# Performance work log

Measured on AMD Instinct MI355X. Metric: run time of the kernel, lower is better.

## Reference

```python
import jax, jax.numpy as jnp
import numpy as np

B, T, E, K, NNEG = 128, 512, 128, 4, 64


def setup_inputs() -> dict:
    key = jax.random.key(0)
    k1, k2, k3, k4 = jax.random.split(key, 4)
    base_payload = jax.random.normal(k1, (B, T, E), dtype=jnp.float32)
    mapped_ctx_payload = jax.random.normal(k2, (B, T, E, K), dtype=jnp.float32)
    seq_lens = jax.random.randint(k3, (B,), 1, T + 1, dtype=jnp.int32)
    # valid positions mask over the flattened (B*T) pool of possible negatives
    valid = (jnp.arange(T)[None, :] < seq_lens[:, None]).reshape(-1)  # [B*T]
    logits = jnp.where(valid, 0.0, -1e30)[None, :]                    # [1, B*T]
    logits = jnp.broadcast_to(logits, (B, B * T))
    # mirrors torch.multinomial(mask, n_negatives): one draw set per batch row
    sample_ids = jax.random.categorical(k4, logits, shape=(NNEG, B)).T.astype(jnp.int32)
    return {
        "base_payload": base_payload,
        "mapped_ctx_payload": mapped_ctx_payload,
        "seq_lens": seq_lens,
        "sample_ids": sample_ids,
    }


def reference(base_payload, mapped_ctx_payload, seq_lens, sample_ids):
    b, t, e = base_payload.shape
    n_steps = mapped_ctx_payload.shape[-1]
    # length mask [b, t]
    len_mask = (jnp.arange(t)[None, :] < seq_lens[:, None]).astype(base_payload.dtype)
    # zero context embeddings past each sequence's length
    trimmed_mce = mapped_ctx_payload * len_mask[:, :, None, None]  # [b, t, e, n_steps]
    # gather sampled negatives from the flattened base embedding pool
    neg_samples = base_payload.reshape(b * t, e)[sample_ids]  # [b, n_neg, e]

    step_losses = []
    for i in range(1, n_steps + 1):
        ce_i = trimmed_mce[:, : t - i, :, i - 1]   # [b, t-i, e]
        be_i = base_payload[:, i:]                  # [b, t-i, e]
        positive_pred = jnp.sum(ce_i * be_i, axis=-1)             # [b, t-i]
        neg_pred = jnp.einsum('bse,bne->bsn', ce_i, neg_samples)  # [b, t-i, n_neg]
        logits = jnp.concatenate([positive_pred[..., None], neg_pred], axis=-1)
        step_losses.append(-jax.nn.log_softmax(logits, axis=-1)[:, :, 0].mean())
    return jnp.stack(step_losses).mean()
```

## Files before the change

### kernel.cpp

```cpp
#include <hip/hip_runtime.h>
#include <math.h>

#define NB 128
#define NT 512
#define NEDIM 128
#define NNEG 64
#define SCHUNK 32
#define NBLK (NB * (NT / SCHUNK))

typedef __bf16 bf16x8 __attribute__((ext_vector_type(8)));
typedef float  f32x4  __attribute__((ext_vector_type(4)));

__launch_bounds__(256, 3)
__global__ void cpc_mfma_kernel(const float* __restrict__ base,
                                const float* __restrict__ mce,
                                const int*  __restrict__ seq_lens,
                                const int*  __restrict__ sample_ids,
                                float* __restrict__ ws)
{
    const int b    = blockIdx.y;
    const int s0   = blockIdx.x * SCHUNK;
    const int slot = b * (NT / SCHUNK) + blockIdx.x;
    const int L    = seq_lens[b];
    const float LOG65 = 4.1743873f;
    const float wgt[4] = {1.f/261632.f, 1.f/261120.f, 1.f/260608.f, 1.f/260096.f};

    if (s0 >= L) {
        if (threadIdx.x == 0) {
            float c = 0.f;
            #pragma unroll
            for (int i = 1; i <= 4; ++i) {
                int hi = min(SCHUNK, (NT - i) - s0);
                if (hi > 0) c += (float)hi * LOG65 * wgt[i - 1];
            }
            ws[slot] = c;
        }
        return;
    }

    __shared__ __bf16 Afrag[2048 * 8];
    __shared__ __bf16 Bfrag[1024 * 8];
    __shared__ float  pos_lds[128];
    __shared__ float  wsum[4];

    const int tid  = threadIdx.x;
    const int lane = tid & 63;
    const int w    = tid >> 6;
    const int q    = lane >> 4;
    const int fl   = lane & 15;

    const float4* mce4 = (const float4*)mce;

    #pragma unroll
    for (int it = 0; it < 2; ++it) {
        int g  = tid + 256 * it;
        int s  = g & 31;
        int eb = g >> 5;
        const float4* src = mce4 + (size_t)(b * NT + s0 + s) * NEDIM + eb * 8;
        float4 v[8];
        #pragma unroll
        for (int u = 0; u < 8; ++u) v[u] = src[u];
        const float* vf = (const float*)v;
        int Cs = (eb >> 2) * 8 + (s >> 2);
        int base_chunk = Cs * 64 + (eb & 3) * 16 + (s & 3) * 4;
        int x = Cs & 7;
        #pragma unroll
        for (int k = 0; k < 4; ++k) {
            int phys = (base_chunk + k) ^ x;
            bf16x8 o;
            #pragma unroll
            for (int u = 0; u < 8; ++u) o[u] = (__bf16)vf[4 * u + k];
            *(bf16x8*)(&Afrag[phys * 8]) = o;
        }
    }

    {
        int n = tid & 63;
        int r = sample_ids[b * NNEG + n];
        const float4* srcb = (const float4*)(base + (size_t)r * NEDIM);
        int eb0 = (tid >> 6) * 4;
        #pragma unroll
        for (int it = 0; it < 4; ++it) {
            int eb = eb0 + it;
            float4 v0 = srcb[eb * 2], v1 = srcb[eb * 2 + 1];
            const float* f0 = (const float*)&v0;
            const float* f1 = (const float*)&v1;
            bf16x8 o;
            #pragma unroll
            for (int u = 0; u < 4; ++u) { o[u] = (__bf16)f0[u]; o[4 + u] = (__bf16)f1[u]; }
            *(bf16x8*)(&Bfrag[(eb * 64 + n) * 8]) = o;
        }
    }
    __syncthreads();

    f32x4 acc[2][4];
    #pragma unroll
    for (int mtl = 0; mtl < 2; ++mtl)
        #pragma unroll
        for (int nt = 0; nt < 4; ++nt) acc[mtl][nt] = (f32x4){0.f, 0.f, 0.f, 0.f};

    #pragma unroll
    for (int kstep = 0; kstep < 4; ++kstep) {
        bf16x8 af[2];
        #pragma unroll
        for (int mtl = 0; mtl < 2; ++mtl) {
            int Cs = kstep * 8 + (2 * w + mtl);
            int phys = (Cs * 64 + lane) ^ (Cs & 7);
            af[mtl] = *(const bf16x8*)(&Afrag[phys * 8]);
        }
        bf16x8 bv[4];
        #pragma unroll
        for (int nt = 0; nt < 4; ++nt) {
            int cB = (kstep * 4 + q) * 64 + nt * 16 + fl;
            bv[nt] = *(const bf16x8*)(&Bfrag[cB * 8]);
        }
        #pragma unroll
        for (int mtl = 0; mtl < 2; ++mtl)
            #pragma unroll
            for (int nt = 0; nt < 4; ++nt)
                acc[mtl][nt] = __builtin_amdgcn_mfma_f32_16x16x32_bf16(
                    af[mtl], bv[nt], acc[mtl][nt], 0, 0, 0);
    }

    {
        int m    = tid >> 1;
        int eh   = tid & 1;
        int sloc = m >> 2, ip = (m & 3) + 1;
        int srow = s0 + sloc + ip; if (srow > NT - 1) srow = NT - 1;
        const float4* brow4 = (const float4*)(base + (size_t)(b * NT + srow) * NEDIM + eh * 64);
        int mt = m >> 4, flm = m & 15;
        float psum = 0.f;
        #pragma unroll
        for (int el = 0; el < 8; ++el) {
            int eb = eh * 8 + el;
            int Cs = (eb >> 2) * 8 + mt;
            int phys = (Cs * 64 + (eb & 3) * 16 + flm) ^ (Cs & 7);
            bf16x8 av = *(const bf16x8*)(&Afrag[phys * 8]);
            float4 b0 = brow4[el * 2], b1 = brow4[el * 2 + 1];
            const float* f0 = (const float*)&b0;
            const float* f1 = (const float*)&b1;
            #pragma unroll
            for (int u = 0; u < 4; ++u) {
                psum = fmaf((float)av[u],     f0[u], psum);
                psum = fmaf((float)av[4 + u], f1[u], psum);
            }
        }
        psum += __shfl_xor(psum, 1);
        if (eh == 0) pos_lds[m] = psum;
    }
    __syncthreads();

    float lossacc = 0.f;
    #pragma unroll
    for (int mtl = 0; mtl < 2; ++mtl) {
        #pragma unroll
        for (int r = 0; r < 4; ++r) {
            int m  = w * 32 + mtl * 16 + q * 4 + r;
            int sg = s0 + (m >> 2);
            int ip = (m & 3) + 1;
            float z0 = acc[mtl][0][r], z1 = acc[mtl][1][r];
            float z2 = acc[mtl][2][r], z3 = acc[mtl][3][r];
            float p  = pos_lds[m];
            float mx = fmaxf(fmaxf(z0, z1), fmaxf(z2, z3));
            mx = fmaxf(mx, __shfl_xor(mx, 1));
            mx = fmaxf(mx, __shfl_xor(mx, 2));
            mx = fmaxf(mx, __shfl_xor(mx, 4));
            mx = fmaxf(mx, __shfl_xor(mx, 8));
            mx = fmaxf(mx, p);
            float es = __expf(z0 - mx) + __expf(z1 - mx)
                     + __expf(z2 - mx) + __expf(z3 - mx);
            es += __shfl_xor(es, 1);
            es += __shfl_xor(es, 2);
            es += __shfl_xor(es, 4);
            es += __shfl_xor(es, 8);
            es += __expf(p - mx);
            float loss = __logf(es) + (mx - p);
            loss = (sg < L) ? loss : LOG65;
            bool take = (sg < NT - ip) && (fl == 0);
            lossacc += take ? wgt[ip - 1] * loss : 0.f;
        }
    }
    lossacc += __shfl_xor(lossacc, 16);
    lossacc += __shfl_xor(lossacc, 32);
    if (lane == 0) wsum[w] = lossacc;
    __syncthreads();
    if (tid == 0) ws[slot] = wsum[0] + wsum[1] + wsum[2] + wsum[3];
}

__global__ void reduce_k(const float* __restrict__ ws, float* __restrict__ out) {
    const int tid = threadIdx.x;
    float s = 0.f;
    #pragma unroll
    for (int i = 0; i < NBLK / 256; ++i) s += ws[tid + 256 * i];
    s += __shfl_xor(s, 1);
    s += __shfl_xor(s, 2);
    s += __shfl_xor(s, 4);
    s += __shfl_xor(s, 8);
    s += __shfl_xor(s, 16);
    s += __shfl_xor(s, 32);
    __shared__ float wsum[4];
    if ((tid & 63) == 0) wsum[tid >> 6] = s;
    __syncthreads();
    if (tid == 0) out[0] = wsum[0] + wsum[1] + wsum[2] + wsum[3];
}

extern "C" void kernel_launch(void* const* d_in, const int* in_sizes, int n_in,
                              void* d_out, int out_size, void* d_ws, size_t ws_size,
                              hipStream_t stream) {
    (void)in_sizes; (void)n_in; (void)out_size; (void)ws_size;
    const float* base       = (const float*)d_in[0];
    const float* mce        = (const float*)d_in[1];
    const int*   seq_lens   = (const int*)d_in[2];
    const int*   sample_ids = (const int*)d_in[3];
    float* out = (float*)d_out;
    float* ws  = (float*)d_ws;

    dim3 grid(NT / SCHUNK, NB);
    cpc_mfma_kernel<<<grid, 256, 0, stream>>>(base, mce, seq_lens, sample_ids, ws);
    reduce_k<<<1, 256, 0, stream>>>(ws, out);
}
```

Measured before the change: 222.8 us.

## Fold positive dot products into MFMA via extra shifted-row B columns

Measured after the change: 211.9 us. 4.9% less time.

```diff
diff --git a/kernel.cpp b/kernel.cpp
--- a/kernel.cpp
+++ b/kernel.cpp
@@ -5,13 +5,15 @@
 #define NT 512
 #define NEDIM 128
 #define NNEG 64
-#define SCHUNK 32
-#define NBLK (NB * (NT / SCHUNK))
+#define SCHUNK 16
+#define NCHUNK (NT / SCHUNK)
+#define NBLK (NB * NCHUNK)
+#define WSN (NBLK * 4)
 
 typedef __bf16 bf16x8 __attribute__((ext_vector_type(8)));
 typedef float  f32x4  __attribute__((ext_vector_type(4)));
 
-__launch_bounds__(256, 3)
+__launch_bounds__(256, 4)
 __global__ void cpc_mfma_kernel(const float* __restrict__ base,
                                 const float* __restrict__ mce,
                                 const int*  __restrict__ seq_lens,
@@ -20,28 +22,26 @@
 {
     const int b    = blockIdx.y;
     const int s0   = blockIdx.x * SCHUNK;
-    const int slot = b * (NT / SCHUNK) + blockIdx.x;
+    const int slot = (b * NCHUNK + blockIdx.x) * 4;
     const int L    = seq_lens[b];
     const float LOG65 = 4.1743873f;
     const float wgt[4] = {1.f/261632.f, 1.f/261120.f, 1.f/260608.f, 1.f/260096.f};
 
     if (s0 >= L) {
-        if (threadIdx.x == 0) {
+        if (threadIdx.x < 4) {
             float c = 0.f;
             #pragma unroll
             for (int i = 1; i <= 4; ++i) {
                 int hi = min(SCHUNK, (NT - i) - s0);
                 if (hi > 0) c += (float)hi * LOG65 * wgt[i - 1];
             }
-            ws[slot] = c;
+            ws[slot + threadIdx.x] = (threadIdx.x == 0) ? c : 0.f;
         }
         return;
     }
 
-    __shared__ __bf16 Afrag[2048 * 8];
-    __shared__ __bf16 Bfrag[1024 * 8];
-    __shared__ float  pos_lds[128];
-    __shared__ float  wsum[4];
+    __shared__ __bf16 Afrag[1024 * 8];
+    __shared__ __bf16 Bfrag[1536 * 8];
 
     const int tid  = threadIdx.x;
     const int lane = tid & 63;
@@ -51,17 +51,15 @@
 
     const float4* mce4 = (const float4*)mce;
 
-    #pragma unroll
-    for (int it = 0; it < 2; ++it) {
-        int g  = tid + 256 * it;
-        int s  = g & 31;
-        int eb = g >> 5;
+    {
+        int s  = tid & 15;
+        int eb = tid >> 4;
         const float4* src = mce4 + (size_t)(b * NT + s0 + s) * NEDIM + eb * 8;
         float4 v[8];
         #pragma unroll
         for (int u = 0; u < 8; ++u) v[u] = src[u];
         const float* vf = (const float*)v;
-        int Cs = (eb >> 2) * 8 + (s >> 2);
+        int Cs = (eb >> 2) * 4 + (s >> 2);
         int base_chunk = Cs * 64 + (eb & 3) * 16 + (s & 3) * 4;
         int x = Cs & 7;
         #pragma unroll
@@ -74,124 +72,103 @@
         }
     }
 
-    {
-        int n = tid & 63;
-        int r = sample_ids[b * NNEG + n];
+    #pragma unroll
+    for (int it = 0; it < 4; ++it) {
+        int h  = tid + 256 * it;
+        int n  = h >> 4;
+        int eb = h & 15;
+        int r  = sample_ids[b * NNEG + n];
         const float4* srcb = (const float4*)(base + (size_t)r * NEDIM);
-        int eb0 = (tid >> 6) * 4;
+        float4 v0 = srcb[eb * 2], v1 = srcb[eb * 2 + 1];
+        const float* f0 = (const float*)&v0;
+        const float* f1 = (const float*)&v1;
+        bf16x8 o;
         #pragma unroll
-        for (int it = 0; it < 4; ++it) {
-            int eb = eb0 + it;
-            float4 v0 = srcb[eb * 2], v1 = srcb[eb * 2 + 1];
+        for (int u = 0; u < 4; ++u) { o[u] = (__bf16)f0[u]; o[4 + u] = (__bf16)f1[u]; }
+        int phys = (eb * 96 + n) ^ (eb & 7);
+        *(bf16x8*)(&Bfrag[phys * 8]) = o;
+    }
+
+    #pragma unroll
+    for (int it = 0; it < 2; ++it) {
+        int h  = tid + 256 * it;
+        int j  = h >> 4;
+        int eb = h & 15;
+        bf16x8 o;
+        #pragma unroll
+        for (int u = 0; u < 8; ++u) o[u] = (__bf16)0.f;
+        if (j < SCHUNK + 3) {
+            int srow = s0 + 1 + j; if (srow > NT - 1) srow = NT - 1;
+            const float4* srcp = (const float4*)(base + (size_t)(b * NT + srow) * NEDIM);
+            float4 v0 = srcp[eb * 2], v1 = srcp[eb * 2 + 1];
             const float* f0 = (const float*)&v0;
             const float* f1 = (const float*)&v1;
-            bf16x8 o;
             #pragma unroll
             for (int u = 0; u < 4; ++u) { o[u] = (__bf16)f0[u]; o[4 + u] = (__bf16)f1[u]; }
-            *(bf16x8*)(&Bfrag[(eb * 64 + n) * 8]) = o;
         }
+        int phys = (eb * 96 + 64 + j) ^ (eb & 7);
+        *(bf16x8*)(&Bfrag[phys * 8]) = o;
     }
     __syncthreads();
 
-    f32x4 acc[2][4];
+    f32x4 acc[6];
     #pragma unroll
-    for (int mtl = 0; mtl < 2; ++mtl)
-        #pragma unroll
-        for (int nt = 0; nt < 4; ++nt) acc[mtl][nt] = (f32x4){0.f, 0.f, 0.f, 0.f};
+    for (int nt = 0; nt < 6; ++nt) acc[nt] = (f32x4){0.f, 0.f, 0.f, 0.f};
 
     #pragma unroll
     for (int kstep = 0; kstep < 4; ++kstep) {
-        bf16x8 af[2];
+        int CsA = kstep * 4 + w;
+        bf16x8 af = *(const bf16x8*)(&Afrag[((CsA * 64 + lane) ^ (CsA & 7)) * 8]);
+        int ebB = kstep * 4 + q;
+        int xb  = ebB & 7;
+        bf16x8 bv[6];
         #pragma unroll
-        for (int mtl = 0; mtl < 2; ++mtl) {
-            int Cs = kstep * 8 + (2 * w + mtl);
-            int phys = (Cs * 64 + lane) ^ (Cs & 7);
-            af[mtl] = *(const bf16x8*)(&Afrag[phys * 8]);
-        }
-        bf16x8 bv[4];
+        for (int nt = 0; nt < 6; ++nt)
+            bv[nt] = *(const bf16x8*)(&Bfrag[((ebB * 96 + nt * 16 + fl) ^ xb) * 8]);
         #pragma unroll
-        for (int nt = 0; nt < 4; ++nt) {
-            int cB = (kstep * 4 + q) * 64 + nt * 16 + fl;
-            bv[nt] = *(const bf16x8*)(&Bfrag[cB * 8]);
-        }
-        #pragma unroll
-        for (int mtl = 0; mtl < 2; ++mtl)
-            #pragma unroll
-            for (int nt = 0; nt < 4; ++nt)
-                acc[mtl][nt] = __builtin_amdgcn_mfma_f32_16x16x32_bf16(
-                    af[mtl], bv[nt], acc[mtl][nt], 0, 0, 0);
+        for (int nt = 0; nt < 6; ++nt)
+            acc[nt] = __builtin_amdgcn_mfma_f32_16x16x32_bf16(af, bv[nt], acc[nt], 0, 0, 0);
     }
 
-    {
-        int m    = tid >> 1;
-        int eh   = tid & 1;
-        int sloc = m >> 2, ip = (m & 3) + 1;
-        int srow = s0 + sloc + ip; if (srow > NT - 1) srow = NT - 1;
-        const float4* brow4 = (const float4*)(base + (size_t)(b * NT + srow) * NEDIM + eh * 64);
-        int mt = m >> 4, flm = m & 15;
-        float psum = 0.f;
-        #pragma unroll
-        for (int el = 0; el < 8; ++el) {
-            int eb = eh * 8 + el;
-            int Cs = (eb >> 2) * 8 + mt;
-            int phys = (Cs * 64 + (eb & 3) * 16 + flm) ^ (Cs & 7);
-            bf16x8 av = *(const bf16x8*)(&Afrag[phys * 8]);
-            float4 b0 = brow4[el * 2], b1 = brow4[el * 2 + 1];
-            const float* f0 = (const float*)&b0;
-            const float* f1 = (const float*)&b1;
-            #pragma unroll
-            for (int u = 0; u < 4; ++u) {
-                psum = fmaf((float)av[u],     f0[u], psum);
-                psum = fmaf((float)av[4 + u], f1[u], psum);
-            }
-        }
-        psum += __shfl_xor(psum, 1);
-        if (eh == 0) pos_lds[m] = psum;
-    }
-    __syncthreads();
-
+    const int sloc = w * 4 + q;
+    const int sg   = s0 + sloc;
     float lossacc = 0.f;
     #pragma unroll
-    for (int mtl = 0; mtl < 2; ++mtl) {
-        #pragma unroll
-        for (int r = 0; r < 4; ++r) {
-            int m  = w * 32 + mtl * 16 + q * 4 + r;
-            int sg = s0 + (m >> 2);
-            int ip = (m & 3) + 1;
-            float z0 = acc[mtl][0][r], z1 = acc[mtl][1][r];
-            float z2 = acc[mtl][2][r], z3 = acc[mtl][3][r];
-            float p  = pos_lds[m];
-            float mx = fmaxf(fmaxf(z0, z1), fmaxf(z2, z3));
-            mx = fmaxf(mx, __shfl_xor(mx, 1));
-            mx = fmaxf(mx, __shfl_xor(mx, 2));
-            mx = fmaxf(mx, __shfl_xor(mx, 4));
-            mx = fmaxf(mx, __shfl_xor(mx, 8));
-            mx = fmaxf(mx, p);
-            float es = __expf(z0 - mx) + __expf(z1 - mx)
-                     + __expf(z2 - mx) + __expf(z3 - mx);
-            es += __shfl_xor(es, 1);
-            es += __shfl_xor(es, 2);
-            es += __shfl_xor(es, 4);
-            es += __shfl_xor(es, 8);
-            es += __expf(p - mx);
-            float loss = __logf(es) + (mx - p);
-            loss = (sg < L) ? loss : LOG65;
-            bool take = (sg < NT - ip) && (fl == 0);
-            lossacc += take ? wgt[ip - 1] * loss : 0.f;
-        }
+    for (int r = 0; r < 4; ++r) {
+        int ip   = r + 1;
+        int pcol = sloc + r;
+        float z0 = acc[0][r], z1 = acc[1][r];
+        float z2 = acc[2][r], z3 = acc[3][r];
+        float pv = (pcol < 16) ? acc[4][r] : acc[5][r];
+        float p  = __shfl(pv, (lane & 48) | (pcol & 15));
+        float mx = fmaxf(fmaxf(z0, z1), fmaxf(z2, z3));
+        mx = fmaxf(mx, __shfl_xor(mx, 1));
+        mx = fmaxf(mx, __shfl_xor(mx, 2));
+        mx = fmaxf(mx, __shfl_xor(mx, 4));
+        mx = fmaxf(mx, __shfl_xor(mx, 8));
+        mx = fmaxf(mx, p);
+        float es = __expf(z0 - mx) + __expf(z1 - mx)
+                 + __expf(z2 - mx) + __expf(z3 - mx);
+        es += __shfl_xor(es, 1);
+        es += __shfl_xor(es, 2);
+        es += __shfl_xor(es, 4);
+        es += __shfl_xor(es, 8);
+        es += __expf(p - mx);
+        float loss = __logf(es) + (mx - p);
+        loss = (sg < L) ? loss : LOG65;
+        bool take = (sg < NT - ip) && (fl == 0);
+        lossacc += take ? wgt[r] * loss : 0.f;
     }
     lossacc += __shfl_xor(lossacc, 16);
     lossacc += __shfl_xor(lossacc, 32);
-    if (lane == 0) wsum[w] = lossacc;
-    __syncthreads();
-    if (tid == 0) ws[slot] = wsum[0] + wsum[1] + wsum[2] + wsum[3];
+    if (lane == 0) ws[slot + w] = lossacc;
 }
 
 __global__ void reduce_k(const float* __restrict__ ws, float* __restrict__ out) {
     const int tid = threadIdx.x;
     float s = 0.f;
     #pragma unroll
-    for (int i = 0; i < NBLK / 256; ++i) s += ws[tid + 256 * i];
+    for (int i = 0; i < WSN / 256; ++i) s += ws[tid + 256 * i];
     s += __shfl_xor(s, 1);
     s += __shfl_xor(s, 2);
     s += __shfl_xor(s, 4);
@@ -215,7 +192,7 @@
     float* out = (float*)d_out;
     float* ws  = (float*)d_ws;
 
-    dim3 grid(NT / SCHUNK, NB);
+    dim3 grid(NCHUNK, NB);
     cpc_mfma_kernel<<<grid, 256, 0, stream>>>(base, mce, seq_lens, sample_ids, ws);
     reduce_k<<<1, 256, 0, stream>>>(ws, out);
 }
```
